# Optimization experiments

Measured on AMD Instinct MI355X. Metric: run time of the kernel, lower is better.

## Reference

```python
import jax, jax.numpy as jnp
import numpy as np

B, T, C = 64, 256, 64
E, H, HB, OUT = 32, 64, 128, 2


def setup_inputs() -> dict:
    key = jax.random.key(0)
    ks = iter(jax.random.split(key, 32))
    s = 0.02
    p = {}
    p["x"] = jax.random.normal(next(ks), (B, T, C), jnp.float32)
    # embedding Linear(1, E)
    p["embed_w"] = jax.random.normal(next(ks), (E, 1), jnp.float32) * s
    p["embed_b"] = jnp.zeros((E,), jnp.float32)
    # GRU (input E, hidden H); gate order r,z,n
    p["w_ih"] = jax.random.normal(next(ks), (3 * H, E), jnp.float32) * s
    p["w_hh"] = jax.random.normal(next(ks), (3 * H, H), jnp.float32) * s
    p["b_ih"] = jnp.zeros((3 * H,), jnp.float32)
    p["b_hh"] = jnp.zeros((3 * H,), jnp.float32)
    # BTP query / key MLPs: H->HB->HB->HB
    for nm in ("q", "k"):
        p[f"{nm}1_w"] = jax.random.normal(next(ks), (HB, H), jnp.float32) * s
        p[f"{nm}1_b"] = jnp.zeros((HB,), jnp.float32)
        p[f"{nm}2_w"] = jax.random.normal(next(ks), (HB, HB), jnp.float32) * s
        p[f"{nm}2_b"] = jnp.zeros((HB,), jnp.float32)
        p[f"{nm}3_w"] = jax.random.normal(next(ks), (HB, HB), jnp.float32) * s
        p[f"{nm}3_b"] = jnp.zeros((HB,), jnp.float32)
    # Gate bias (n_components x n_components), torch.randn init
    p["gate_bias"] = jax.random.normal(next(ks), (C, C), jnp.float32)
    # classifier: C^2 -> C^2/2 -> C^2/4 -> OUT
    d0, d1, d2 = C * C, C * C // 2, C * C // 4
    p["clf1_w"] = jax.random.normal(next(ks), (d1, d0), jnp.float32) * s
    p["clf1_b"] = jnp.zeros((d1,), jnp.float32)
    p["clf2_w"] = jax.random.normal(next(ks), (d2, d1), jnp.float32) * s
    p["clf2_b"] = jnp.zeros((d2,), jnp.float32)
    p["clf3_w"] = jax.random.normal(next(ks), (OUT, d2), jnp.float32) * s
    p["clf3_b"] = jnp.zeros((OUT,), jnp.float32)
    # predictor Linear(H, 1)
    p["pred_w"] = jax.random.normal(next(ks), (1, H), jnp.float32) * s
    p["pred_b"] = jnp.zeros((1,), jnp.float32)
    return p


def _mlp3(h, w1, b1, w2, b2, w3, b3):
    h = jax.nn.relu(h @ w1.T + b1)
    h = jax.nn.relu(h @ w2.T + b2)
    return h @ w3.T + b3


def reference(x, embed_w, embed_b, w_ih, w_hh, b_ih, b_hh,
              q1_w, q1_b, q2_w, q2_b, q3_w, q3_b,
              k1_w, k1_b, k2_w, k2_b, k3_w, k3_b,
              gate_bias, clf1_w, clf1_b, clf2_w, clf2_b, clf3_w, clf3_b,
              pred_w, pred_b):
    Bb, Tt, Cc = x.shape
    Hh = w_hh.shape[1]
    # embeddings: Linear(1,E) applied to each scalar -> [B,C,T,E]
    embedded = x.transpose(0, 2, 1)[..., None] * embed_w[:, 0] + embed_b
    xs = jnp.moveaxis(embedded, 2, 0)  # [T,B,C,E]

    def gru_cell(h, xt):
        gi = xt @ w_ih.T + b_ih           # [B,C,3H]
        gh = h @ w_hh.T + b_hh
        gi_r, gi_z, gi_n = jnp.split(gi, 3, axis=-1)
        gh_r, gh_z, gh_n = jnp.split(gh, 3, axis=-1)
        r = jax.nn.sigmoid(gi_r + gh_r)
        z = jax.nn.sigmoid(gi_z + gh_z)
        n = jnp.tanh(gi_n + r * gh_n)
        return (1.0 - z) * n + z * h

    def btp(h):
        q = _mlp3(h, q1_w, q1_b, q2_w, q2_b, q3_w, q3_b)   # [B,C,HB]
        k = _mlp3(h, k1_w, k1_b, k2_w, k2_b, k3_w, k3_b)
        transfer = jnp.einsum('bqd,bkd->bqk', q, k)        # [B,C,C]
        norms = jnp.sqrt(jnp.sum(transfer * transfer, axis=(1, 2), keepdims=True))
        transfer = transfer / norms
        gate = jax.nn.sigmoid(jnp.abs(transfer) + gate_bias)
        transfer = transfer * gate
        next_states = jnp.einsum('bij,bjd->bid', transfer, h)
        return next_states, transfer

    def step(h, xt):
        h = gru_cell(h, xt)
        h, transfer = btp(h)
        return h, (h, transfer)

    h0 = jnp.zeros((Bb, Cc, Hh), x.dtype)
    _, (hs, mats) = jax.lax.scan(step, h0, xs)
    hidden_states = jnp.moveaxis(hs, 0, 1)    # [B,T,C,H]
    matrices = jnp.moveaxis(mats, 0, 1)       # [B,T,C,C]

    # predictor on hidden states at t=0..T-2 -> predicts x[:,1:,:]
    predicted = (hidden_states[:, :-1] @ pred_w.T + pred_b)[..., 0]  # [B,T-1,C]

    clf_in = matrices.reshape(Bb, Tt, Cc * Cc)
    h1 = jax.nn.relu(clf_in @ clf1_w.T + clf1_b)   # dropout is identity in eval
    h2 = jax.nn.relu(h1 @ clf2_w.T + clf2_b)
    time_logits = h2 @ clf3_w.T + clf3_b            # [B,T,OUT]
    logits = jnp.mean(time_logits, axis=1)          # [B,OUT]
    return logits, matrices, time_logits, predicted, x[:, 1:, :]
```

## Files before the change

kernel.cpp:

```cpp
#include <hip/hip_runtime.h>
#include <hip/hip_bf16.h>
#include <math.h>

#define B_BATCH 64
#define T_STEPS 256
#define C_COMP  64

#define WSW_BYTE_OFF 2048
#define WHH_OFF 0
#define Q1_OFF 12288
#define K1_OFF 20480
#define Q2_OFF 28672
#define K2_OFF 45056
#define Q3_OFF 61440
#define K3_OFF 77824
#define C1WB_BYTE 262144
#define C2WB_BYTE 17039360
#define H1B_BYTE  21233664
#define H2B_BYTE  88342528
#define MB16_BYTE 121896960ULL

#define MAT_OFF  128
#define TL_OFF   67108992
#define PRED_OFF 67141760
#define XC_OFF   68186240

#define GST 196
#define HS  68
#define TS  68
#define GBS 68

typedef __attribute__((ext_vector_type(8))) short short8;
typedef __attribute__((ext_vector_type(4))) float f32x4;
#define MFMA16(a,b,c) __builtin_amdgcn_mfma_f32_16x16x32_bf16(a,b,c,0,0,0)

__device__ __forceinline__ float fsigm(float v) {
    return __builtin_amdgcn_rcpf(1.0f + __expf(-v));
}
__device__ __forceinline__ float ftanh(float v) {
    return 1.0f - 2.0f * __builtin_amdgcn_rcpf(__expf(2.0f * v) + 1.0f);
}
__device__ __forceinline__ short f2bs(float f) {
    unsigned u = __float_as_uint(f);
    u += 0x7fffu + ((u >> 16) & 1u);
    return (short)(u >> 16);
}
__device__ __forceinline__ float bf2f(short s) {
    return __uint_as_float(((unsigned)(unsigned short)s) << 16);
}
__device__ __forceinline__ unsigned pk2(float a, float b) {
    return (unsigned)(unsigned short)f2bs(a) | ((unsigned)(unsigned short)f2bs(b) << 16);
}
__device__ __forceinline__ void bar_lds() {
    asm volatile("s_waitcnt lgkmcnt(0)" ::: "memory");
    __builtin_amdgcn_s_barrier();
}
__device__ __forceinline__ int xorr(int row) { return ((row >> 1) & 7) << 3; }

__device__ __forceinline__ void async16(void* lds, const void* g) {
    __builtin_amdgcn_global_load_lds((const __attribute__((address_space(1))) void*)g,
                                     (__attribute__((address_space(3))) void*)lds, 16, 0, 0);
}

__global__ void precompute_kernel(const float* __restrict__ w_ih,
                                  const float* __restrict__ embed_w,
                                  const float* __restrict__ embed_b,
                                  const float* __restrict__ b_ih,
                                  float* __restrict__ avec, float* __restrict__ cvec)
{
    int g = threadIdx.x;
    if (g < 192) {
        float a = 0.f, c = 0.f;
        for (int e = 0; e < 32; ++e) {
            float w = w_ih[g * 32 + e];
            a += w * embed_w[e];
            c += w * embed_b[e];
        }
        avec[g] = a;
        cvec[g] = c + b_ih[g];
    }
}

__global__ void tobf16_kernel(const float* __restrict__ src, short* __restrict__ dst, int n)
{
    int i = blockIdx.x * 256 + threadIdx.x;
    if (i < n) dst[i] = f2bs(src[i]);
}

__global__ void expand_kernel(const short* __restrict__ mb, float* __restrict__ mat)
{
    const size_t i = ((size_t)blockIdx.x * 256 + threadIdx.x) * 8;
    short8 v = *(const short8*)&mb[i];
    float4 lo, hi;
    lo.x = bf2f(v[0]); lo.y = bf2f(v[1]); lo.z = bf2f(v[2]); lo.w = bf2f(v[3]);
    hi.x = bf2f(v[4]); hi.y = bf2f(v[5]); hi.z = bf2f(v[6]); hi.w = bf2f(v[7]);
    *reinterpret_cast<float4*>(&mat[i])     = lo;
    *reinterpret_cast<float4*>(&mat[i + 4]) = hi;
}

template<int KST, int AST, bool RELU>
__device__ __forceinline__ void two_strip_sw(
    const short* __restrict__ A,
    const short8* __restrict__ B0, const short8* __restrict__ B1,
    const f32x4 bias0, const f32x4 bias1,
    short* __restrict__ outb, const int s0, const int s1, const int ln, const int lh)
{
    f32x4 acc0[4], acc1[4];
#pragma unroll
    for (int g = 0; g < 4; ++g) { acc0[g] = bias0; acc1[g] = bias1; }
#pragma unroll
    for (int kk = 0; kk < KST; ++kk)
#pragma unroll
        for (int g = 0; g < 4; ++g) {
            const int row = g * 16 + ln;
            short8 a = *(const short8*)&A[row * AST + ((kk * 32 + lh * 8) ^ xorr(row))];
            acc0[g] = MFMA16(B0[kk], a, acc0[g]);
            acc1[g] = MFMA16(B1[kk], a, acc1[g]);
        }
#pragma unroll
    for (int g = 0; g < 4; ++g) {
        const int row = g * 16 + ln;
        f32x4 v0 = acc0[g], v1 = acc1[g];
        if (RELU) {
#pragma unroll
            for (int q = 0; q < 4; ++q) { v0[q] = fmaxf(v0[q], 0.f); v1[q] = fmaxf(v1[q], 0.f); }
        }
        uint2 p0, p1;
        p0.x = pk2(v0[0], v0[1]); p0.y = pk2(v0[2], v0[3]);
        p1.x = pk2(v1[0], v1[1]); p1.y = pk2(v1[2], v1[3]);
        *(uint2*)&outb[row * 128 + ((s0 * 16 + lh * 4) ^ xorr(row))] = p0;
        *(uint2*)&outb[row * 128 + ((s1 * 16 + lh * 4) ^ xorr(row))] = p1;
    }
}

__global__ __launch_bounds__(512) void scan_kernel(
    const float* __restrict__ x, const float* __restrict__ b_hh,
    const float* __restrict__ avec, const float* __restrict__ cvec,
    const short* __restrict__ wsw,
    const float* __restrict__ q1b, const float* __restrict__ q2b, const float* __restrict__ q3b,
    const float* __restrict__ k1b, const float* __restrict__ k2b, const float* __restrict__ k3b,
    const float* __restrict__ gate_bias,
    const float* __restrict__ pred_w, const float* __restrict__ pred_b,
    float* __restrict__ matrices, float* __restrict__ predicted,
    short* __restrict__ mb16, const int use_mb16)
{
    __shared__ __align__(16) short hb  [64 * 64];
    __shared__ __align__(16) short hbN [64 * 64];
    __shared__ __align__(16) short hbT [64 * 64];
    __shared__ __align__(16) float h32 [64 * HS];
    __shared__ __align__(16) short qf  [64 * 128];
    __shared__ __align__(16) short kf  [64 * 128];
    __shared__ __align__(16) float gbias_s[64 * GBS];
    __shared__ __align__(16) char arena[65536];
    __shared__ __align__(16) float avec_s[192];
    __shared__ __align__(16) float cvec_s[192];
    __shared__ __align__(16) float bhh_s[192];
    __shared__ __align__(16) float pw_s[64];
    __shared__ __align__(16) float xrow[64];
    __shared__ __align__(16) float red[8];

    float* gates = (float*)arena;
    short* act2q = (short*)arena;
    short* act2k = (short*)(arena + 16384);
    short* act1q = (short*)(arena + 32768);
    short* act1k = (short*)(arena + 49152);
    float* tf    = (float*)arena;
    short* tb    = (short*)(arena + 20480);

    const int tid = threadIdx.x;
    const int b = blockIdx.x;
    const int w = tid >> 6, lane = tid & 63;
    const int ln = lane & 15, lh = lane >> 4;
    const int path = w >> 2;
    const int wq = w & 3;

    for (int i = tid; i < 64 * 64; i += 512) { hb[i] = 0; hbN[i] = 0; hbT[i] = 0; }
    for (int i = tid; i < 64 * HS; i += 512) h32[i] = 0.f;
    for (int i = tid; i < 4096; i += 512)
        gbias_s[(i >> 6) * GBS + (i & 63)] = gate_bias[i];
    if (tid < 192) { avec_s[tid] = avec[tid]; cvec_s[tid] = cvec[tid]; bhh_s[tid] = b_hh[tid]; }
    if (tid < 64) { pw_s[tid] = pred_w[tid]; xrow[tid] = x[(size_t)b * T_STEPS * 64 + tid]; }
    const float pbv = pred_b[0];

    const short* whh_b = wsw + WHH_OFF;
    const short* l1w = path ? wsw + K1_OFF : wsw + Q1_OFF;
    const short* l2w = path ? wsw + K2_OFF : wsw + Q2_OFF;
    const short* l3w = path ? wsw + K3_OFF : wsw + Q3_OFF;
    const float* l1b = path ? k1b : q1b;
    const float* l2b = path ? k2b : q2b;
    const float* l3b = path ? k3b : q3b;

    short8 Bg[2][2], B1[2][2], B2[2][4], B3[2][4];
#pragma unroll
    for (int kk = 0; kk < 2; ++kk)
        Bg[0][kk] = *(const short8*)&whh_b[(w * 16 + ln) * 64 + kk * 32 + lh * 8];
    if (w < 4) {
#pragma unroll
        for (int kk = 0; kk < 2; ++kk)
            Bg[1][kk] = *(const short8*)&whh_b[((w + 8) * 16 + ln) * 64 + kk * 32 + lh * 8];
    }
#pragma unroll
    for (int s = 0; s < 2; ++s) {
        const int strip = wq + s * 4;
#pragma unroll
        for (int kk = 0; kk < 2; ++kk)
            B1[s][kk] = *(const short8*)&l1w[(strip * 16 + ln) * 64 + kk * 32 + lh * 8];
#pragma unroll
        for (int kk = 0; kk < 4; ++kk) {
            B2[s][kk] = *(const short8*)&l2w[(strip * 16 + ln) * 128 + kk * 32 + lh * 8];
            B3[s][kk] = *(const short8*)&l3w[(strip * 16 + ln) * 128 + kk * 32 + lh * 8];
        }
    }
    const f32x4 b1v0 = *(const f32x4*)&l1b[wq * 16 + lh * 4];
    const f32x4 b1v1 = *(const f32x4*)&l1b[(wq + 4) * 16 + lh * 4];
    const f32x4 b2v0 = *(const f32x4*)&l2b[wq * 16 + lh * 4];
    const f32x4 b2v1 = *(const f32x4*)&l2b[(wq + 4) * 16 + lh * 4];
    const f32x4 b3v0 = *(const f32x4*)&l3b[wq * 16 + lh * 4];
    const f32x4 b3v1 = *(const f32x4*)&l3b[(wq + 4) * 16 + lh * 4];
    __syncthreads();

    for (int t = 0; t < T_STEPS; ++t) {
        float xnext = 0.f;
        if (tid < 64 && t + 1 < T_STEPS)
            xnext = x[((size_t)b * T_STEPS + t + 1) * 64 + tid];
        if (t > 0) {
            const int c = tid >> 3, j0 = (tid & 7) * 8;
            f32x4 h0 = *(const f32x4*)&h32[c * HS + j0];
            f32x4 h1 = *(const f32x4*)&h32[c * HS + j0 + 4];
            f32x4 w0 = *(const f32x4*)&pw_s[j0];
            f32x4 w1 = *(const f32x4*)&pw_s[j0 + 4];
            float p = 0.f;
#pragma unroll
            for (int q = 0; q < 4; ++q) p = fmaf(h0[q], w0[q], fmaf(h1[q], w1[q], p));
            p += __shfl_xor(p, 1); p += __shfl_xor(p, 2); p += __shfl_xor(p, 4);
            if ((lane & 7) == 0)
                predicted[((size_t)b * (T_STEPS - 1) + (t - 1)) * 64 + c] = p + pbv;
        }
        {
            f32x4 accA[4], accB[4];
            const f32x4 bhA = *(const f32x4*)&bhh_s[w * 16 + lh * 4];
#pragma unroll
            for (int g = 0; g < 4; ++g) accA[g] = bhA;
            if (w < 4) {
                const f32x4 bhB = *(const f32x4*)&bhh_s[(w + 8) * 16 + lh * 4];
#pragma unroll
                for (int g = 0; g < 4; ++g) accB[g] = bhB;
            }
#pragma unroll
            for (int kk = 0; kk < 2; ++kk)
#pragma unroll
                for (int g = 0; g < 4; ++g) {
                    const int row = g * 16 + ln;
                    short8 hv = *(const short8*)&hb[row * 64 + ((kk * 32 + lh * 8) ^ xorr(row))];
                    accA[g] = MFMA16(Bg[0][kk], hv, accA[g]);
                    if (w < 4) accB[g] = MFMA16(Bg[1][kk], hv, accB[g]);
                }
#pragma unroll
            for (int g = 0; g < 4; ++g)
                *(f32x4*)&gates[(g * 16 + ln) * GST + w * 16 + lh * 4] = accA[g];
            if (w < 4) {
#pragma unroll
                for (int g = 0; g < 4; ++g)
                    *(f32x4*)&gates[(g * 16 + ln) * GST + (w + 8) * 16 + lh * 4] = accB[g];
            }
        }
        bar_lds();

        {
            const int c = tid >> 3, j0 = (tid & 7) * 8;
            const float xv = xrow[c];
            unsigned pk[4];
#pragma unroll
            for (int h2 = 0; h2 < 2; ++h2) {
                const int jh = j0 + h2 * 4;
                f32x4 gr4 = *(const f32x4*)&gates[c * GST + jh];
                f32x4 gz4 = *(const f32x4*)&gates[c * GST + 64 + jh];
                f32x4 gn4 = *(const f32x4*)&gates[c * GST + 128 + jh];
                f32x4 ho4 = *(const f32x4*)&h32[c * HS + jh];
                f32x4 ar4 = *(const f32x4*)&avec_s[jh];
                f32x4 az4 = *(const f32x4*)&avec_s[64 + jh];
                f32x4 an4 = *(const f32x4*)&avec_s[128 + jh];
                f32x4 cr4 = *(const f32x4*)&cvec_s[jh];
                f32x4 cz4 = *(const f32x4*)&cvec_s[64 + jh];
                f32x4 cn4 = *(const f32x4*)&cvec_s[128 + jh];
                f32x4 hn4;
#pragma unroll
                for (int q = 0; q < 4; ++q) {
                    const float r = fsigm(gr4[q] + fmaf(xv, ar4[q], cr4[q]));
                    const float z = fsigm(gz4[q] + fmaf(xv, az4[q], cz4[q]));
                    const float n = ftanh(fmaf(r, gn4[q], fmaf(xv, an4[q], cn4[q])));
                    hn4[q] = fmaf(z, ho4[q] - n, n);
                }
                *(f32x4*)&h32[c * HS + jh] = hn4;
                const unsigned plo = pk2(hn4[0], hn4[1]);
                const unsigned phi = pk2(hn4[2], hn4[3]);
                pk[h2 * 2] = plo; pk[h2 * 2 + 1] = phi;
                hbT[(jh + 0) * 64 + (c ^ xorr(jh + 0))] = (short)plo;
                hbT[(jh + 1) * 64 + (c ^ xorr(jh + 1))] = (short)(plo >> 16);
                hbT[(jh + 2) * 64 + (c ^ xorr(jh + 2))] = (short)phi;
                hbT[(jh + 3) * 64 + (c ^ xorr(jh + 3))] = (short)(phi >> 16);
            }
            uint4 pv; pv.x = pk[0]; pv.y = pk[1]; pv.z = pk[2]; pv.w = pk[3];
            *(uint4*)&hbN[c * 64 + (j0 ^ xorr(c))] = pv;
        }
        bar_lds();

        two_strip_sw<2, 64,  true >(hbN, B1[0], B1[1], b1v0, b1v1,
                                    path ? act1k : act1q, wq, wq + 4, ln, lh);
        bar_lds();
        two_strip_sw<4, 128, true >(path ? act1k : act1q, B2[0], B2[1], b2v0, b2v1,
                                    path ? act2k : act2q, wq, wq + 4, ln, lh);
        bar_lds();
        two_strip_sw<4, 128, false>(path ? act2k : act2q, B3[0], B3[1], b3v0, b3v1,
                                    path ? kf : qf, wq, wq + 4, ln, lh);
        bar_lds();

        {
            const int qg = w & 3, kg = (w >> 2) * 2;
            f32x4 ac0 = {0,0,0,0}, ac1 = {0,0,0,0};
#pragma unroll
            for (int kk = 0; kk < 4; ++kk) {
                const int rq = qg * 16 + ln, rk0 = kg * 16 + ln, rk1 = (kg + 1) * 16 + ln;
                short8 bq = *(const short8*)&qf[rq * 128 + ((kk * 32 + lh * 8) ^ xorr(rq))];
                short8 a0 = *(const short8*)&kf[rk0 * 128 + ((kk * 32 + lh * 8) ^ xorr(rk0))];
                short8 a1 = *(const short8*)&kf[rk1 * 128 + ((kk * 32 + lh * 8) ^ xorr(rk1))];
                ac0 = MFMA16(a0, bq, ac0);
                ac1 = MFMA16(a1, bq, ac1);
            }
            const int qrow = qg * 16 + ln;
            *(f32x4*)&tf[qrow * TS + kg * 16 + lh * 4]       = ac0;
            *(f32x4*)&tf[qrow * TS + (kg + 1) * 16 + lh * 4] = ac1;
            float ss = 0.f;
#pragma unroll
            for (int q = 0; q < 4; ++q)
                ss = fmaf(ac0[q], ac0[q], fmaf(ac1[q], ac1[q], ss));
#pragma unroll
            for (int off = 1; off < 64; off <<= 1) ss += __shfl_xor(ss, off);
            if (lane == 0) red[w] = ss;
            if (tid < 64 && t + 1 < T_STEPS) xrow[tid] = xnext;
        }
        bar_lds();

        {
            const int ci = tid >> 3, j0 = (tid & 7) * 8;
            const float ssum = red[0]+red[1]+red[2]+red[3]+red[4]+red[5]+red[6]+red[7];
            const float inv = __builtin_amdgcn_rsqf(ssum);
            const size_t mbase = ((size_t)b * T_STEPS + t) * 4096;
            unsigned pk[4];
#pragma unroll
            for (int h2 = 0; h2 < 2; ++h2) {
                const int jh = j0 + h2 * 4;
                f32x4 t4  = *(const f32x4*)&tf[ci * TS + jh];
                f32x4 gb4 = *(const f32x4*)&gbias_s[ci * GBS + jh];
                f32x4 v4;
#pragma unroll
                for (int q = 0; q < 4; ++q) {
                    const float tv = t4[q] * inv;
                    const float g = fsigm(fabsf(tv) + gb4[q]);
                    v4[q] = tv * g;
                }
                pk[h2 * 2]     = pk2(v4[0], v4[1]);
                pk[h2 * 2 + 1] = pk2(v4[2], v4[3]);
                if (!use_mb16)
                    *(f32x4*)&matrices[mbase + ci * 64 + jh] = v4;
            }
            uint4 pv; pv.x = pk[0]; pv.y = pk[1]; pv.z = pk[2]; pv.w = pk[3];
            if (use_mb16)
                *(uint4*)&mb16[mbase + ci * 64 + j0] = pv;
            *(uint4*)&tb[ci * 64 + (j0 ^ xorr(ci))] = pv;
        }
        bar_lds();

        {
            const int jg = w & 3, ig = (w >> 2) * 2;
            f32x4 hc0 = {0,0,0,0}, hc1 = {0,0,0,0};
#pragma unroll
            for (int kk = 0; kk < 2; ++kk) {
                const int rj = jg * 16 + ln, ri0 = ig * 16 + ln, ri1 = (ig + 1) * 16 + ln;
                short8 bt = *(const short8*)&tb [rj * 64 + ((kk * 32 + lh * 8) ^ xorr(rj))];
                short8 a0 = *(const short8*)&hbT[ri0 * 64 + ((kk * 32 + lh * 8) ^ xorr(ri0))];
                short8 a1 = *(const short8*)&hbT[ri1 * 64 + ((kk * 32 + lh * 8) ^ xorr(ri1))];
                hc0 = MFMA16(a0, bt, hc0);
                hc1 = MFMA16(a1, bt, hc1);
            }
            const int row = jg * 16 + ln;
            *(f32x4*)&h32[row * HS + ig * 16 + lh * 4]       = hc0;
            *(f32x4*)&h32[row * HS + (ig + 1) * 16 + lh * 4] = hc1;
            uint2 p0, p1;
            p0.x = pk2(hc0[0], hc0[1]); p0.y = pk2(hc0[2], hc0[3]);
            p1.x = pk2(hc1[0], hc1[1]); p1.y = pk2(hc1[2], hc1[3]);
            *(uint2*)&hb[row * 64 + ((ig * 16 + lh * 4) ^ xorr(row))]       = p0;
            *(uint2*)&hb[row * 64 + (((ig + 1) * 16 + lh * 4) ^ xorr(row))] = p1;
        }
        bar_lds();
    }
}

__global__ void copyx_kernel(const float* __restrict__ x, float* __restrict__ out5)
{
    int i = blockIdx.x * 256 + threadIdx.x;
    if (i < B_BATCH * (T_STEPS - 1) * C_COMP) {
        int b = i / ((T_STEPS - 1) * C_COMP);
        int r = i - b * (T_STEPS - 1) * C_COMP;
        out5[i] = x[(size_t)b * (T_STEPS * C_COMP) + r + C_COMP];
    }
}

__global__ __launch_bounds__(256) void gemm1_kernel(
    const float* __restrict__ A, const short* __restrict__ Bw,
    const float* __restrict__ bias, short* __restrict__ Cb,
    const int M, const int N, const int K)
{
    __shared__ __align__(16) short Asb[128 * 64];
    __shared__ __align__(16) short Bsb[128 * 64];
    const int tid = threadIdx.x;
    const int w = tid >> 6, lane = tid & 63;
    const int ln = lane & 15, lh = lane >> 4;
    const int wr = w >> 1, wc = w & 1;

    const int ntc = N >> 7;
    const int g = blockIdx.x;
    const int xcd = g & 7, chunk = g >> 3;
    const int mt = xcd * ((M >> 7) >> 3) + chunk / ntc;
    const int nt = chunk % ntc;
    const int m0 = mt << 7, n0 = nt << 7;

    const int ar = tid >> 1;
    const int ac = (tid & 1) << 5;
    const short* bsrc = Bw + (size_t)(n0 + w * 32 + (lane >> 3)) * K + ((lane & 7) << 3);
    short* bdst = &Bsb[w * 32 * 64 + lane * 8];

    f32x4 acc[4][4];
#pragma unroll
    for (int m = 0; m < 4; ++m)
#pragma unroll
        for (int n = 0; n < 4; ++n) acc[m][n] = (f32x4){0, 0, 0, 0};

    for (int k0 = 0; k0 < K; k0 += 64) {
        const float* arow = A + (size_t)(m0 + ar) * K + k0 + ac;
        float4 av[8];
#pragma unroll
        for (int i = 0; i < 8; ++i) av[i] = *reinterpret_cast<const float4*>(arow + i * 4);
        short8 cv[4];
#pragma unroll
        for (int i = 0; i < 4; ++i) {
            cv[i][0] = f2bs(av[2*i].x);   cv[i][1] = f2bs(av[2*i].y);
            cv[i][2] = f2bs(av[2*i].z);   cv[i][3] = f2bs(av[2*i].w);
            cv[i][4] = f2bs(av[2*i+1].x); cv[i][5] = f2bs(av[2*i+1].y);
            cv[i][6] = f2bs(av[2*i+1].z); cv[i][7] = f2bs(av[2*i+1].w);
        }
        __syncthreads();
#pragma unroll
        for (int i = 0; i < 4; ++i)
            *reinterpret_cast<short8*>(&Asb[ar * 64 + ac + i * 8]) = cv[i];
#pragma unroll
        for (int i = 0; i < 4; ++i)
            async16(bdst + i * 512, bsrc + (size_t)i * 8 * K + k0);
        __syncthreads();
#pragma unroll
        for (int kk = 0; kk < 2; ++kk) {
            short8 af[4], bfr[4];
#pragma unroll
            for (int m = 0; m < 4; ++m)
                af[m] = *reinterpret_cast<const short8*>(&Asb[(wr*64 + m*16 + ln)*64 + kk*32 + lh*8]);
#pragma unroll
            for (int n = 0; n < 4; ++n)
                bfr[n] = *reinterpret_cast<const short8*>(&Bsb[(wc*64 + n*16 + ln)*64 + kk*32 + lh*8]);
#pragma unroll
            for (int m = 0; m < 4; ++m)
#pragma unroll
                for (int n = 0; n < 4; ++n)
                    acc[m][n] = MFMA16(af[m], bfr[n], acc[m][n]);
        }
    }
#pragma unroll
    for (int n = 0; n < 4; ++n) {
        const int col = n0 + wc * 64 + n * 16 + ln;
        const float bv = bias[col];
#pragma unroll
        for (int m = 0; m < 4; ++m)
#pragma unroll
            for (int q = 0; q < 4; ++q) {
                const int row = m0 + wr * 64 + m * 16 + lh * 4 + q;
                Cb[(size_t)row * N + col] = f2bs(fmaxf(acc[m][n][q] + bv, 0.f));
            }
    }
}

__global__ __launch_bounds__(256) void gemm2_kernel(
    const short* __restrict__ Ab, const short* __restrict__ Bw,
    const float* __restrict__ bias, short* __restrict__ Cb,
    const int M, const int N, const int K)
{
    __shared__ __align__(16) short Asb[128 * 64];
    __shared__ __align__(16) short Bsb[128 * 64];
    const int tid = threadIdx.x;
    const int w = tid >> 6, lane = tid & 63;
    const int ln = lane & 15, lh = lane >> 4;
    const int wr = w >> 1, wc = w & 1;

    const int ntc = N >> 7;
    const int g = blockIdx.x;
    const int xcd = g & 7, chunk = g >> 3;
    const int mt = xcd * ((M >> 7) >> 3) + chunk / ntc;
    const int nt = chunk % ntc;
    const int m0 = mt << 7, n0 = nt << 7;

    const short* asrc = Ab + (size_t)(m0 + w * 32 + (lane >> 3)) * K + ((lane & 7) << 3);
    const short* bsrc = Bw + (size_t)(n0 + w * 32 + (lane >> 3)) * K + ((lane & 7) << 3);
    short* adst = &Asb[w * 32 * 64 + lane * 8];
    short* bdst = &Bsb[w * 32 * 64 + lane * 8];

    f32x4 acc[4][4];
#pragma unroll
    for (int m = 0; m < 4; ++m)
#pragma unroll
        for (int n = 0; n < 4; ++n) acc[m][n] = (f32x4){0, 0, 0, 0};

    for (int k0 = 0; k0 < K; k0 += 64) {
        __syncthreads();
#pragma unroll
        for (int i = 0; i < 4; ++i) {
            async16(adst + i * 512, asrc + (size_t)i * 8 * K + k0);
            async16(bdst + i * 512, bsrc + (size_t)i * 8 * K + k0);
        }
        __syncthreads();
#pragma unroll
        for (int kk = 0; kk < 2; ++kk) {
            short8 af[4], bfr[4];
#pragma unroll
            for (int m = 0; m < 4; ++m)
                af[m] = *reinterpret_cast<const short8*>(&Asb[(wr*64 + m*16 + ln)*64 + kk*32 + lh*8]);
#pragma unroll
            for (int n = 0; n < 4; ++n)
                bfr[n] = *reinterpret_cast<const short8*>(&Bsb[(wc*64 + n*16 + ln)*64 + kk*32 + lh*8]);
#pragma unroll
            for (int m = 0; m < 4; ++m)
#pragma unroll
                for (int n = 0; n < 4; ++n)
                    acc[m][n] = MFMA16(af[m], bfr[n], acc[m][n]);
        }
    }
#pragma unroll
    for (int n = 0; n < 4; ++n) {
        const int col = n0 + wc * 64 + n * 16 + ln;
        const float bv = bias[col];
#pragma unroll
        for (int m = 0; m < 4; ++m)
#pragma unroll
            for (int q = 0; q < 4; ++q) {
                const int row = m0 + wr * 64 + m * 16 + lh * 4 + q;
                Cb[(size_t)row * N + col] = f2bs(fmaxf(acc[m][n][q] + bv, 0.f));
            }
    }
}

__global__ __launch_bounds__(256) void clf3_kernel(const short* __restrict__ h2b,
    const float* __restrict__ w3, const float* __restrict__ b3, float* __restrict__ TL)
{
    const int lane = threadIdx.x & 63;
    const int w = threadIdx.x >> 6;
    const size_t r = (size_t)blockIdx.x * 4 + w;
    const short* hr = h2b + r * 1024;
    float a0 = 0.f, a1 = 0.f;
#pragma unroll
    for (int half = 0; half < 2; ++half) {
        const int k = half * 512 + lane * 8;
        short8 hv = *(const short8*)&hr[k];
#pragma unroll
        for (int u = 0; u < 8; ++u) {
            const float hf = bf2f(hv[u]);
            a0 = fmaf(hf, w3[k + u], a0);
            a1 = fmaf(hf, w3[1024 + k + u], a1);
        }
    }
    for (int off = 32; off; off >>= 1) { a0 += __shfl_xor(a0, off); a1 += __shfl_xor(a1, off); }
    if (lane == 0) {
        TL[r * 2 + 0] = a0 + b3[0];
        TL[r * 2 + 1] = a1 + b3[1];
    }
}

__global__ void logits_kernel(const float* __restrict__ TL, float* __restrict__ out)
{
    const int tid = threadIdx.x;
    if (tid >= 128) return;
    const int b = tid >> 1, o = tid & 1;
    float s = 0.f;
    for (int t = 0; t < T_STEPS; ++t) s += TL[((size_t)b * T_STEPS + t) * 2 + o];
    out[b * 2 + o] = s * (1.0f / 256.0f);
}

extern "C" void kernel_launch(void* const* d_in, const int* in_sizes, int n_in,
                              void* d_out, int out_size, void* d_ws, size_t ws_size,
                              hipStream_t stream)
{
    const float* x       = (const float*)d_in[0];
    const float* embed_w = (const float*)d_in[1];
    const float* embed_b = (const float*)d_in[2];
    const float* w_ih    = (const float*)d_in[3];
    const float* w_hh    = (const float*)d_in[4];
    const float* b_ih    = (const float*)d_in[5];
    const float* b_hh    = (const float*)d_in[6];
    const float* q1w = (const float*)d_in[7],  *q1b = (const float*)d_in[8];
    const float* q2w = (const float*)d_in[9],  *q2b = (const float*)d_in[10];
    const float* q3w = (const float*)d_in[11], *q3b = (const float*)d_in[12];
    const float* k1w = (const float*)d_in[13], *k1b = (const float*)d_in[14];
    const float* k2w = (const float*)d_in[15], *k2b = (const float*)d_in[16];
    const float* k3w = (const float*)d_in[17], *k3b = (const float*)d_in[18];
    const float* gate_bias = (const float*)d_in[19];
    const float* c1w = (const float*)d_in[20], *c1b = (const float*)d_in[21];
    const float* c2w = (const float*)d_in[22], *c2b = (const float*)d_in[23];
    const float* c3w = (const float*)d_in[24], *c3b = (const float*)d_in[25];
    const float* pw  = (const float*)d_in[26], *pb  = (const float*)d_in[27];

    float* out       = (float*)d_out;
    float* logits    = out;
    float* matrices  = out + MAT_OFF;
    float* TL        = out + TL_OFF;
    float* predicted = out + PRED_OFF;
    float* xcopy     = out + XC_OFF;

    float* ws   = (float*)d_ws;
    float* avec = ws;
    float* cvec = ws + 192;
    short* wsw  = (short*)((char*)d_ws + WSW_BYTE_OFF);
    short* c1wb = (short*)((char*)d_ws + C1WB_BYTE);
    short* c2wb = (short*)((char*)d_ws + C2WB_BYTE);
    short* h1b  = (short*)((char*)d_ws + H1B_BYTE);
    short* h2b  = (short*)((char*)d_ws + H2B_BYTE);

    const int use_mb16 = (ws_size >= MB16_BYTE + 134217728ULL) ? 1 : 0;
    short* mb16 = use_mb16 ? (short*)((char*)d_ws + MB16_BYTE) : (short*)d_ws;

    precompute_kernel<<<1, 256, 0, stream>>>(w_ih, embed_w, embed_b, b_ih, avec, cvec);

    tobf16_kernel<<<(12288 + 255) / 256, 256, 0, stream>>>(w_hh, wsw + WHH_OFF, 12288);
    tobf16_kernel<<<(8192  + 255) / 256, 256, 0, stream>>>(q1w,  wsw + Q1_OFF,  8192);
    tobf16_kernel<<<(8192  + 255) / 256, 256, 0, stream>>>(k1w,  wsw + K1_OFF,  8192);
    tobf16_kernel<<<(16384 + 255) / 256, 256, 0, stream>>>(q2w,  wsw + Q2_OFF,  16384);
    tobf16_kernel<<<(16384 + 255) / 256, 256, 0, stream>>>(k2w,  wsw + K2_OFF,  16384);
    tobf16_kernel<<<(16384 + 255) / 256, 256, 0, stream>>>(q3w,  wsw + Q3_OFF,  16384);
    tobf16_kernel<<<(16384 + 255) / 256, 256, 0, stream>>>(k3w,  wsw + K3_OFF,  16384);
    tobf16_kernel<<<(2048 * 4096 + 255) / 256, 256, 0, stream>>>(c1w, c1wb, 2048 * 4096);
    tobf16_kernel<<<(1024 * 2048 + 255) / 256, 256, 0, stream>>>(c2w, c2wb, 1024 * 2048);

    scan_kernel<<<B_BATCH, 512, 0, stream>>>(x, b_hh, avec, cvec, wsw,
        q1b, q2b, q3b, k1b, k2b, k3b, gate_bias, pw, pb, matrices, predicted,
        mb16, use_mb16);

    if (use_mb16)
        expand_kernel<<<32768, 256, 0, stream>>>(mb16, matrices);

    copyx_kernel<<<(B_BATCH * (T_STEPS - 1) * C_COMP + 255) / 256, 256, 0, stream>>>(x, xcopy);

    const int Mtot = B_BATCH * T_STEPS;
    if (use_mb16) {
        gemm2_kernel<<<(Mtot / 128) * (2048 / 128), 256, 0, stream>>>(
            mb16, c1wb, c1b, h1b, Mtot, 2048, 4096);
    } else {
        gemm1_kernel<<<(Mtot / 128) * (2048 / 128), 256, 0, stream>>>(
            matrices, c1wb, c1b, h1b, Mtot, 2048, 4096);
    }
    gemm2_kernel<<<(Mtot / 128) * (1024 / 128), 256, 0, stream>>>(
        h1b, c2wb, c2b, h2b, Mtot, 1024, 2048);
    clf3_kernel<<<Mtot / 4, 256, 0, stream>>>(h2b, c3w, c3b, TL);
    logits_kernel<<<1, 128, 0, stream>>>(TL, logits);
}
```

Measured before the change: 2.770 ms.

## Fuse scan and classifier GEMMs into persistent kernel with atomic job queue

```diff
diff --git a/kernel.cpp b/kernel.cpp
--- a/kernel.cpp
+++ b/kernel.cpp
@@ -6,7 +6,8 @@
 #define T_STEPS 256
 #define C_COMP  64
 
-#define WSW_BYTE_OFF 2048
+#define CTRL_BYTE 2048
+#define WSW_BYTE_OFF 4096
 #define WHH_OFF 0
 #define Q1_OFF 12288
 #define K1_OFF 20480
@@ -30,6 +31,8 @@
 #define TS  68
 #define GBS 68
 
+#define NJOB 3328
+
 typedef __attribute__((ext_vector_type(8))) short short8;
 typedef __attribute__((ext_vector_type(4))) float f32x4;
 #define MFMA16(a,b,c) __builtin_amdgcn_mfma_f32_16x16x32_bf16(a,b,c,0,0,0)
@@ -60,6 +63,24 @@
 __device__ __forceinline__ void async16(void* lds, const void* g) {
     __builtin_amdgcn_global_load_lds((const __attribute__((address_space(1))) void*)g,
                                      (__attribute__((address_space(3))) void*)lds, 16, 0, 0);
+}
+__device__ __forceinline__ int aload_acq(int* p) {
+    return __hip_atomic_load(p, __ATOMIC_ACQUIRE, __HIP_MEMORY_SCOPE_AGENT);
+}
+__device__ __forceinline__ void astore_rel(int* p, int v) {
+    __hip_atomic_store(p, v, __ATOMIC_RELEASE, __HIP_MEMORY_SCOPE_AGENT);
+}
+__device__ __forceinline__ int aadd_rel(int* p, int v) {
+    return __hip_atomic_fetch_add(p, v, __ATOMIC_RELEASE, __HIP_MEMORY_SCOPE_AGENT);
+}
+__device__ __forceinline__ int aadd_rlx(int* p, int v) {
+    return __hip_atomic_fetch_add(p, v, __ATOMIC_RELAXED, __HIP_MEMORY_SCOPE_AGENT);
+}
+__device__ __forceinline__ void wait_ge(int* p, int need) {
+    if (threadIdx.x == 0) {
+        while (aload_acq(p) < need) __builtin_amdgcn_s_sleep(127);
+    }
+    __syncthreads();
 }
 
 __global__ void precompute_kernel(const float* __restrict__ w_ih,
@@ -98,6 +119,101 @@
     *reinterpret_cast<float4*>(&mat[i + 4]) = hi;
 }
 
+__global__ void copyx_kernel(const float* __restrict__ x, float* __restrict__ out5)
+{
+    int i = blockIdx.x * 256 + threadIdx.x;
+    if (i < B_BATCH * (T_STEPS - 1) * C_COMP) {
+        int b = i / ((T_STEPS - 1) * C_COMP);
+        int r = i - b * (T_STEPS - 1) * C_COMP;
+        out5[i] = x[(size_t)b * (T_STEPS * C_COMP) + r + C_COMP];
+    }
+}
+
+template<bool AF32>
+__device__ __forceinline__ void gemm_tile_512(
+    const void* Aptr, const short* __restrict__ Bw, const float* __restrict__ bias,
+    short* __restrict__ Cb, const size_t row0, const int n0,
+    const int N, const int K, short* Asb, short* Bsb)
+{
+    const int tid = threadIdx.x;
+    const int w = tid >> 6, lane = tid & 63;
+    const int ln = lane & 15, lh = lane >> 4;
+    const int wr = w >> 2, wc = w & 3;
+
+    const short* Ab = (const short*)Aptr;
+    const float* Af = (const float*)Aptr;
+
+    f32x4 acc[4][2];
+#pragma unroll
+    for (int m = 0; m < 4; ++m) {
+        acc[m][0] = (f32x4){0, 0, 0, 0};
+        acc[m][1] = (f32x4){0, 0, 0, 0};
+    }
+
+    for (int k0 = 0; k0 < K; k0 += 64) {
+        if (AF32) {
+            const int ar = tid >> 2, ac = (tid & 3) << 4;
+            const float* arow = Af + (row0 + ar) * (size_t)K + k0 + ac;
+            float4 av[4];
+#pragma unroll
+            for (int i = 0; i < 4; ++i) av[i] = *reinterpret_cast<const float4*>(arow + i * 4);
+            short8 cv[2];
+#pragma unroll
+            for (int i = 0; i < 2; ++i) {
+                cv[i][0] = f2bs(av[2*i].x);   cv[i][1] = f2bs(av[2*i].y);
+                cv[i][2] = f2bs(av[2*i].z);   cv[i][3] = f2bs(av[2*i].w);
+                cv[i][4] = f2bs(av[2*i+1].x); cv[i][5] = f2bs(av[2*i+1].y);
+                cv[i][6] = f2bs(av[2*i+1].z); cv[i][7] = f2bs(av[2*i+1].w);
+            }
+            __syncthreads();
+            *reinterpret_cast<short8*>(&Asb[ar * 64 + ac])     = cv[0];
+            *reinterpret_cast<short8*>(&Asb[ar * 64 + ac + 8]) = cv[1];
+#pragma unroll
+            for (int i = 0; i < 2; ++i)
+                async16(&Bsb[w * 1024 + i * 512 + lane * 8],
+                        Bw + (size_t)(n0 + w * 16 + i * 8 + (lane >> 3)) * K + k0 + ((lane & 7) << 3));
+            __syncthreads();
+        } else {
+            __syncthreads();
+#pragma unroll
+            for (int i = 0; i < 2; ++i) {
+                async16(&Asb[w * 1024 + i * 512 + lane * 8],
+                        Ab + (row0 + w * 16 + i * 8 + (lane >> 3)) * (size_t)K + k0 + ((lane & 7) << 3));
+                async16(&Bsb[w * 1024 + i * 512 + lane * 8],
+                        Bw + (size_t)(n0 + w * 16 + i * 8 + (lane >> 3)) * K + k0 + ((lane & 7) << 3));
+            }
+            __syncthreads();
+        }
+#pragma unroll
+        for (int kk = 0; kk < 2; ++kk) {
+            short8 af[4], bfr[2];
+#pragma unroll
+            for (int m = 0; m < 4; ++m)
+                af[m] = *reinterpret_cast<const short8*>(&Asb[(wr*64 + m*16 + ln)*64 + kk*32 + lh*8]);
+#pragma unroll
+            for (int n = 0; n < 2; ++n)
+                bfr[n] = *reinterpret_cast<const short8*>(&Bsb[(wc*32 + n*16 + ln)*64 + kk*32 + lh*8]);
+#pragma unroll
+            for (int m = 0; m < 4; ++m)
+#pragma unroll
+                for (int n = 0; n < 2; ++n)
+                    acc[m][n] = MFMA16(af[m], bfr[n], acc[m][n]);
+        }
+    }
+#pragma unroll
+    for (int n = 0; n < 2; ++n) {
+        const int col = n0 + wc * 32 + n * 16 + ln;
+        const float bv = bias[col];
+#pragma unroll
+        for (int m = 0; m < 4; ++m)
+#pragma unroll
+            for (int q = 0; q < 4; ++q) {
+                const size_t row = row0 + wr * 64 + m * 16 + lh * 4 + q;
+                Cb[row * N + col] = f2bs(fmaxf(acc[m][n][q] + bv, 0.f));
+            }
+    }
+}
+
 template<int KST, int AST, bool RELU>
 __device__ __forceinline__ void two_strip_sw(
     const short* __restrict__ A,
@@ -133,7 +249,7 @@
     }
 }
 
-__global__ __launch_bounds__(512) void scan_kernel(
+__global__ __launch_bounds__(512) void fused_kernel(
     const float* __restrict__ x, const float* __restrict__ b_hh,
     const float* __restrict__ avec, const float* __restrict__ cvec,
     const short* __restrict__ wsw,
@@ -142,7 +258,12 @@
     const float* __restrict__ gate_bias,
     const float* __restrict__ pred_w, const float* __restrict__ pred_b,
     float* __restrict__ matrices, float* __restrict__ predicted,
-    short* __restrict__ mb16, const int use_mb16)
+    short* __restrict__ mb16, const int use_mb16,
+    const short* __restrict__ c1wb, const float* __restrict__ c1b,
+    const short* __restrict__ c2wb, const float* __restrict__ c2b,
+    const float* __restrict__ c3w, const float* __restrict__ c3b,
+    short* __restrict__ h1b, short* __restrict__ h2b, float* __restrict__ TL,
+    int* __restrict__ ctrl, const int persist)
 {
     __shared__ __align__(16) short hb  [64 * 64];
     __shared__ __align__(16) short hbN [64 * 64];
@@ -158,251 +279,328 @@
     __shared__ __align__(16) float pw_s[64];
     __shared__ __align__(16) float xrow[64];
     __shared__ __align__(16) float red[8];
-
-    float* gates = (float*)arena;
-    short* act2q = (short*)arena;
-    short* act2k = (short*)(arena + 16384);
-    short* act1q = (short*)(arena + 32768);
-    short* act1k = (short*)(arena + 49152);
-    float* tf    = (float*)arena;
-    short* tb    = (short*)(arena + 20480);
+    __shared__ int jslot;
 
     const int tid = threadIdx.x;
-    const int b = blockIdx.x;
+    const int bid = blockIdx.x;
     const int w = tid >> 6, lane = tid & 63;
     const int ln = lane & 15, lh = lane >> 4;
-    const int path = w >> 2;
-    const int wq = w & 3;
-
-    for (int i = tid; i < 64 * 64; i += 512) { hb[i] = 0; hbN[i] = 0; hbT[i] = 0; }
-    for (int i = tid; i < 64 * HS; i += 512) h32[i] = 0.f;
-    for (int i = tid; i < 4096; i += 512)
-        gbias_s[(i >> 6) * GBS + (i & 63)] = gate_bias[i];
-    if (tid < 192) { avec_s[tid] = avec[tid]; cvec_s[tid] = cvec[tid]; bhh_s[tid] = b_hh[tid]; }
-    if (tid < 64) { pw_s[tid] = pred_w[tid]; xrow[tid] = x[(size_t)b * T_STEPS * 64 + tid]; }
-    const float pbv = pred_b[0];
-
-    const short* whh_b = wsw + WHH_OFF;
-    const short* l1w = path ? wsw + K1_OFF : wsw + Q1_OFF;
-    const short* l2w = path ? wsw + K2_OFF : wsw + Q2_OFF;
-    const short* l3w = path ? wsw + K3_OFF : wsw + Q3_OFF;
-    const float* l1b = path ? k1b : q1b;
-    const float* l2b = path ? k2b : q2b;
-    const float* l3b = path ? k3b : q3b;
-
-    short8 Bg[2][2], B1[2][2], B2[2][4], B3[2][4];
-#pragma unroll
-    for (int kk = 0; kk < 2; ++kk)
-        Bg[0][kk] = *(const short8*)&whh_b[(w * 16 + ln) * 64 + kk * 32 + lh * 8];
-    if (w < 4) {
+
+    int* qhead = ctrl;
+    int* prog  = ctrl + 16;
+    int* done1 = ctrl + 96;
+    int* done2 = ctrl + 224;
+
+    if (bid < 64) {
+        float* gates = (float*)arena;
+        short* act2q = (short*)arena;
+        short* act2k = (short*)(arena + 16384);
+        short* act1q = (short*)(arena + 32768);
+        short* act1k = (short*)(arena + 49152);
+        float* tf    = (float*)arena;
+        short* tb    = (short*)(arena + 20480);
+
+        const int b = bid;
+        const int path = w >> 2;
+        const int wq = w & 3;
+
+        for (int i = tid; i < 64 * 64; i += 512) { hb[i] = 0; hbN[i] = 0; hbT[i] = 0; }
+        for (int i = tid; i < 64 * HS; i += 512) h32[i] = 0.f;
+        for (int i = tid; i < 4096; i += 512)
+            gbias_s[(i >> 6) * GBS + (i & 63)] = gate_bias[i];
+        if (tid < 192) { avec_s[tid] = avec[tid]; cvec_s[tid] = cvec[tid]; bhh_s[tid] = b_hh[tid]; }
+        if (tid < 64) { pw_s[tid] = pred_w[tid]; xrow[tid] = x[(size_t)b * T_STEPS * 64 + tid]; }
+        const float pbv = pred_b[0];
+
+        const short* whh_b = wsw + WHH_OFF;
+        const short* l1w = path ? wsw + K1_OFF : wsw + Q1_OFF;
+        const short* l2w = path ? wsw + K2_OFF : wsw + Q2_OFF;
+        const short* l3w = path ? wsw + K3_OFF : wsw + Q3_OFF;
+        const float* l1b = path ? k1b : q1b;
+        const float* l2b = path ? k2b : q2b;
+        const float* l3b = path ? k3b : q3b;
+
+        short8 Bg[2][2], B1[2][2], B2[2][4], B3[2][4];
 #pragma unroll
         for (int kk = 0; kk < 2; ++kk)
-            Bg[1][kk] = *(const short8*)&whh_b[((w + 8) * 16 + ln) * 64 + kk * 32 + lh * 8];
-    }
-#pragma unroll
-    for (int s = 0; s < 2; ++s) {
-        const int strip = wq + s * 4;
-#pragma unroll
-        for (int kk = 0; kk < 2; ++kk)
-            B1[s][kk] = *(const short8*)&l1w[(strip * 16 + ln) * 64 + kk * 32 + lh * 8];
-#pragma unroll
-        for (int kk = 0; kk < 4; ++kk) {
-            B2[s][kk] = *(const short8*)&l2w[(strip * 16 + ln) * 128 + kk * 32 + lh * 8];
-            B3[s][kk] = *(const short8*)&l3w[(strip * 16 + ln) * 128 + kk * 32 + lh * 8];
-        }
-    }
-    const f32x4 b1v0 = *(const f32x4*)&l1b[wq * 16 + lh * 4];
-    const f32x4 b1v1 = *(const f32x4*)&l1b[(wq + 4) * 16 + lh * 4];
-    const f32x4 b2v0 = *(const f32x4*)&l2b[wq * 16 + lh * 4];
-    const f32x4 b2v1 = *(const f32x4*)&l2b[(wq + 4) * 16 + lh * 4];
-    const f32x4 b3v0 = *(const f32x4*)&l3b[wq * 16 + lh * 4];
-    const f32x4 b3v1 = *(const f32x4*)&l3b[(wq + 4) * 16 + lh * 4];
-    __syncthreads();
-
-    for (int t = 0; t < T_STEPS; ++t) {
-        float xnext = 0.f;
-        if (tid < 64 && t + 1 < T_STEPS)
-            xnext = x[((size_t)b * T_STEPS + t + 1) * 64 + tid];
-        if (t > 0) {
-            const int c = tid >> 3, j0 = (tid & 7) * 8;
-            f32x4 h0 = *(const f32x4*)&h32[c * HS + j0];
-            f32x4 h1 = *(const f32x4*)&h32[c * HS + j0 + 4];
-            f32x4 w0 = *(const f32x4*)&pw_s[j0];
-            f32x4 w1 = *(const f32x4*)&pw_s[j0 + 4];
-            float p = 0.f;
-#pragma unroll
-            for (int q = 0; q < 4; ++q) p = fmaf(h0[q], w0[q], fmaf(h1[q], w1[q], p));
-            p += __shfl_xor(p, 1); p += __shfl_xor(p, 2); p += __shfl_xor(p, 4);
-            if ((lane & 7) == 0)
-                predicted[((size_t)b * (T_STEPS - 1) + (t - 1)) * 64 + c] = p + pbv;
-        }
-        {
-            f32x4 accA[4], accB[4];
-            const f32x4 bhA = *(const f32x4*)&bhh_s[w * 16 + lh * 4];
-#pragma unroll
-            for (int g = 0; g < 4; ++g) accA[g] = bhA;
-            if (w < 4) {
-                const f32x4 bhB = *(const f32x4*)&bhh_s[(w + 8) * 16 + lh * 4];
-#pragma unroll
-                for (int g = 0; g < 4; ++g) accB[g] = bhB;
-            }
+            Bg[0][kk] = *(const short8*)&whh_b[(w * 16 + ln) * 64 + kk * 32 + lh * 8];
+        if (w < 4) {
 #pragma unroll
             for (int kk = 0; kk < 2; ++kk)
-#pragma unroll
-                for (int g = 0; g < 4; ++g) {
-                    const int row = g * 16 + ln;
-                    short8 hv = *(const short8*)&hb[row * 64 + ((kk * 32 + lh * 8) ^ xorr(row))];
-                    accA[g] = MFMA16(Bg[0][kk], hv, accA[g]);
-                    if (w < 4) accB[g] = MFMA16(Bg[1][kk], hv, accB[g]);
+                Bg[1][kk] = *(const short8*)&whh_b[((w + 8) * 16 + ln) * 64 + kk * 32 + lh * 8];
+        }
+#pragma unroll
+        for (int s = 0; s < 2; ++s) {
+            const int strip = wq + s * 4;
+#pragma unroll
+            for (int kk = 0; kk < 2; ++kk)
+                B1[s][kk] = *(const short8*)&l1w[(strip * 16 + ln) * 64 + kk * 32 + lh * 8];
+#pragma unroll
+            for (int kk = 0; kk < 4; ++kk) {
+                B2[s][kk] = *(const short8*)&l2w[(strip * 16 + ln) * 128 + kk * 32 + lh * 8];
+                B3[s][kk] = *(const short8*)&l3w[(strip * 16 + ln) * 128 + kk * 32 + lh * 8];
+            }
+        }
+        const f32x4 b1v0 = *(const f32x4*)&l1b[wq * 16 + lh * 4];
+        const f32x4 b1v1 = *(const f32x4*)&l1b[(wq + 4) * 16 + lh * 4];
+        const f32x4 b2v0 = *(const f32x4*)&l2b[wq * 16 + lh * 4];
+        const f32x4 b2v1 = *(const f32x4*)&l2b[(wq + 4) * 16 + lh * 4];
+        const f32x4 b3v0 = *(const f32x4*)&l3b[wq * 16 + lh * 4];
+        const f32x4 b3v1 = *(const f32x4*)&l3b[(wq + 4) * 16 + lh * 4];
+        __syncthreads();
+
+        for (int t = 0; t < T_STEPS; ++t) {
+            float xnext = 0.f;
+            if (tid < 64 && t + 1 < T_STEPS)
+                xnext = x[((size_t)b * T_STEPS + t + 1) * 64 + tid];
+            if (t > 0) {
+                const int c = tid >> 3, j0 = (tid & 7) * 8;
+                f32x4 h0 = *(const f32x4*)&h32[c * HS + j0];
+                f32x4 h1 = *(const f32x4*)&h32[c * HS + j0 + 4];
+                f32x4 w0 = *(const f32x4*)&pw_s[j0];
+                f32x4 w1 = *(const f32x4*)&pw_s[j0 + 4];
+                float p = 0.f;
+#pragma unroll
+                for (int q = 0; q < 4; ++q) p = fmaf(h0[q], w0[q], fmaf(h1[q], w1[q], p));
+                p += __shfl_xor(p, 1); p += __shfl_xor(p, 2); p += __shfl_xor(p, 4);
+                if ((lane & 7) == 0)
+                    predicted[((size_t)b * (T_STEPS - 1) + (t - 1)) * 64 + c] = p + pbv;
+            }
+            {
+                f32x4 accA[4], accB[4];
+                const f32x4 bhA = *(const f32x4*)&bhh_s[w * 16 + lh * 4];
+#pragma unroll
+                for (int g = 0; g < 4; ++g) accA[g] = bhA;
+                if (w < 4) {
+                    const f32x4 bhB = *(const f32x4*)&bhh_s[(w + 8) * 16 + lh * 4];
+#pragma unroll
+                    for (int g = 0; g < 4; ++g) accB[g] = bhB;
                 }
 #pragma unroll
-            for (int g = 0; g < 4; ++g)
-                *(f32x4*)&gates[(g * 16 + ln) * GST + w * 16 + lh * 4] = accA[g];
-            if (w < 4) {
+                for (int kk = 0; kk < 2; ++kk)
+#pragma unroll
+                    for (int g = 0; g < 4; ++g) {
+                        const int row = g * 16 + ln;
+                        short8 hv = *(const short8*)&hb[row * 64 + ((kk * 32 + lh * 8) ^ xorr(row))];
+                        accA[g] = MFMA16(Bg[0][kk], hv, accA[g]);
+                        if (w < 4) accB[g] = MFMA16(Bg[1][kk], hv, accB[g]);
+                    }
 #pragma unroll
                 for (int g = 0; g < 4; ++g)
-                    *(f32x4*)&gates[(g * 16 + ln) * GST + (w + 8) * 16 + lh * 4] = accB[g];
-            }
-        }
-        bar_lds();
-
-        {
-            const int c = tid >> 3, j0 = (tid & 7) * 8;
-            const float xv = xrow[c];
-            unsigned pk[4];
-#pragma unroll
-            for (int h2 = 0; h2 < 2; ++h2) {
-                const int jh = j0 + h2 * 4;
-                f32x4 gr4 = *(const f32x4*)&gates[c * GST + jh];
-                f32x4 gz4 = *(const f32x4*)&gates[c * GST + 64 + jh];
-                f32x4 gn4 = *(const f32x4*)&gates[c * GST + 128 + jh];
-                f32x4 ho4 = *(const f32x4*)&h32[c * HS + jh];
-                f32x4 ar4 = *(const f32x4*)&avec_s[jh];
-                f32x4 az4 = *(const f32x4*)&avec_s[64 + jh];
-                f32x4 an4 = *(const f32x4*)&avec_s[128 + jh];
-                f32x4 cr4 = *(const f32x4*)&cvec_s[jh];
-                f32x4 cz4 = *(const f32x4*)&cvec_s[64 + jh];
-                f32x4 cn4 = *(const f32x4*)&cvec_s[128 + jh];
-                f32x4 hn4;
-#pragma unroll
-                for (int q = 0; q < 4; ++q) {
-                    const float r = fsigm(gr4[q] + fmaf(xv, ar4[q], cr4[q]));
-                    const float z = fsigm(gz4[q] + fmaf(xv, az4[q], cz4[q]));
-                    const float n = ftanh(fmaf(r, gn4[q], fmaf(xv, an4[q], cn4[q])));
-                    hn4[q] = fmaf(z, ho4[q] - n, n);
+                    *(f32x4*)&gates[(g * 16 + ln) * GST + w * 16 + lh * 4] = accA[g];
+                if (w < 4) {
+#pragma unroll
+                    for (int g = 0; g < 4; ++g)
+                        *(f32x4*)&gates[(g * 16 + ln) * GST + (w + 8) * 16 + lh * 4] = accB[g];
                 }
-                *(f32x4*)&h32[c * HS + jh] = hn4;
-                const unsigned plo = pk2(hn4[0], hn4[1]);
-                const unsigned phi = pk2(hn4[2], hn4[3]);
-                pk[h2 * 2] = plo; pk[h2 * 2 + 1] = phi;
-                hbT[(jh + 0) * 64 + (c ^ xorr(jh + 0))] = (short)plo;
-                hbT[(jh + 1) * 64 + (c ^ xorr(jh + 1))] = (short)(plo >> 16);
-                hbT[(jh + 2) * 64 + (c ^ xorr(jh + 2))] = (short)phi;
-                hbT[(jh + 3) * 64 + (c ^ xorr(jh + 3))] = (short)(phi >> 16);
-            }
-            uint4 pv; pv.x = pk[0]; pv.y = pk[1]; pv.z = pk[2]; pv.w = pk[3];
-            *(uint4*)&hbN[c * 64 + (j0 ^ xorr(c))] = pv;
-        }
-        bar_lds();
-
-        two_strip_sw<2, 64,  true >(hbN, B1[0], B1[1], b1v0, b1v1,
-                                    path ? act1k : act1q, wq, wq + 4, ln, lh);
-        bar_lds();
-        two_strip_sw<4, 128, true >(path ? act1k : act1q, B2[0], B2[1], b2v0, b2v1,
-                                    path ? act2k : act2q, wq, wq + 4, ln, lh);
-        bar_lds();
-        two_strip_sw<4, 128, false>(path ? act2k : act2q, B3[0], B3[1], b3v0, b3v1,
-                                    path ? kf : qf, wq, wq + 4, ln, lh);
-        bar_lds();
-
-        {
-            const int qg = w & 3, kg = (w >> 2) * 2;
-            f32x4 ac0 = {0,0,0,0}, ac1 = {0,0,0,0};
-#pragma unroll
-            for (int kk = 0; kk < 4; ++kk) {
-                const int rq = qg * 16 + ln, rk0 = kg * 16 + ln, rk1 = (kg + 1) * 16 + ln;
-                short8 bq = *(const short8*)&qf[rq * 128 + ((kk * 32 + lh * 8) ^ xorr(rq))];
-                short8 a0 = *(const short8*)&kf[rk0 * 128 + ((kk * 32 + lh * 8) ^ xorr(rk0))];
-                short8 a1 = *(const short8*)&kf[rk1 * 128 + ((kk * 32 + lh * 8) ^ xorr(rk1))];
-                ac0 = MFMA16(a0, bq, ac0);
-                ac1 = MFMA16(a1, bq, ac1);
-            }
-            const int qrow = qg * 16 + ln;
-            *(f32x4*)&tf[qrow * TS + kg * 16 + lh * 4]       = ac0;
-            *(f32x4*)&tf[qrow * TS + (kg + 1) * 16 + lh * 4] = ac1;
-            float ss = 0.f;
-#pragma unroll
-            for (int q = 0; q < 4; ++q)
-                ss = fmaf(ac0[q], ac0[q], fmaf(ac1[q], ac1[q], ss));
-#pragma unroll
-            for (int off = 1; off < 64; off <<= 1) ss += __shfl_xor(ss, off);
-            if (lane == 0) red[w] = ss;
-            if (tid < 64 && t + 1 < T_STEPS) xrow[tid] = xnext;
-        }
-        bar_lds();
-
-        {
-            const int ci = tid >> 3, j0 = (tid & 7) * 8;
-            const float ssum = red[0]+red[1]+red[2]+red[3]+red[4]+red[5]+red[6]+red[7];
-            const float inv = __builtin_amdgcn_rsqf(ssum);
-            const size_t mbase = ((size_t)b * T_STEPS + t) * 4096;
-            unsigned pk[4];
-#pragma unroll
-            for (int h2 = 0; h2 < 2; ++h2) {
-                const int jh = j0 + h2 * 4;
-                f32x4 t4  = *(const f32x4*)&tf[ci * TS + jh];
-                f32x4 gb4 = *(const f32x4*)&gbias_s[ci * GBS + jh];
-                f32x4 v4;
-#pragma unroll
-                for (int q = 0; q < 4; ++q) {
-                    const float tv = t4[q] * inv;
-                    const float g = fsigm(fabsf(tv) + gb4[q]);
-                    v4[q] = tv * g;
+            }
+            bar_lds();
+
+            {
+                const int c = tid >> 3, j0 = (tid & 7) * 8;
+                const float xv = xrow[c];
+                unsigned pk[4];
+#pragma unroll
+                for (int h2 = 0; h2 < 2; ++h2) {
+                    const int jh = j0 + h2 * 4;
+                    f32x4 gr4 = *(const f32x4*)&gates[c * GST + jh];
+                    f32x4 gz4 = *(const f32x4*)&gates[c * GST + 64 + jh];
+                    f32x4 gn4 = *(const f32x4*)&gates[c * GST + 128 + jh];
+                    f32x4 ho4 = *(const f32x4*)&h32[c * HS + jh];
+                    f32x4 ar4 = *(const f32x4*)&avec_s[jh];
+                    f32x4 az4 = *(const f32x4*)&avec_s[64 + jh];
+                    f32x4 an4 = *(const f32x4*)&avec_s[128 + jh];
+                    f32x4 cr4 = *(const f32x4*)&cvec_s[jh];
+                    f32x4 cz4 = *(const f32x4*)&cvec_s[64 + jh];
+                    f32x4 cn4 = *(const f32x4*)&cvec_s[128 + jh];
+                    f32x4 hn4;
+#pragma unroll
+                    for (int q = 0; q < 4; ++q) {
+                        const float r = fsigm(gr4[q] + fmaf(xv, ar4[q], cr4[q]));
+                        const float z = fsigm(gz4[q] + fmaf(xv, az4[q], cz4[q]));
+                        const float n = ftanh(fmaf(r, gn4[q], fmaf(xv, an4[q], cn4[q])));
+                        hn4[q] = fmaf(z, ho4[q] - n, n);
+                    }
+                    *(f32x4*)&h32[c * HS + jh] = hn4;
+                    const unsigned plo = pk2(hn4[0], hn4[1]);
+                    const unsigned phi = pk2(hn4[2], hn4[3]);
+                    pk[h2 * 2] = plo; pk[h2 * 2 + 1] = phi;
+                    hbT[(jh + 0) * 64 + (c ^ xorr(jh + 0))] = (short)plo;
+                    hbT[(jh + 1) * 64 + (c ^ xorr(jh + 1))] = (short)(plo >> 16);
+                    hbT[(jh + 2) * 64 + (c ^ xorr(jh + 2))] = (short)phi;
+                    hbT[(jh + 3) * 64 + (c ^ xorr(jh + 3))] = (short)(phi >> 16);
                 }
-                pk[h2 * 2]     = pk2(v4[0], v4[1]);
-                pk[h2 * 2 + 1] = pk2(v4[2], v4[3]);
-                if (!use_mb16)
-                    *(f32x4*)&matrices[mbase + ci * 64 + jh] = v4;
-            }
-            uint4 pv; pv.x = pk[0]; pv.y = pk[1]; pv.z = pk[2]; pv.w = pk[3];
+                uint4 pv; pv.x = pk[0]; pv.y = pk[1]; pv.z = pk[2]; pv.w = pk[3];
+                *(uint4*)&hbN[c * 64 + (j0 ^ xorr(c))] = pv;
+            }
+            bar_lds();
+
+            two_strip_sw<2, 64,  true >(hbN, B1[0], B1[1], b1v0, b1v1,
+                                        path ? act1k : act1q, wq, wq + 4, ln, lh);
+            bar_lds();
+            two_strip_sw<4, 128, true >(path ? act1k : act1q, B2[0], B2[1], b2v0, b2v1,
+                                        path ? act2k : act2q, wq, wq + 4, ln, lh);
+            bar_lds();
+            two_strip_sw<4, 128, false>(path ? act2k : act2q, B3[0], B3[1], b3v0, b3v1,
+                                        path ? kf : qf, wq, wq + 4, ln, lh);
+            bar_lds();
+
+            {
+                const int qg = w & 3, kg = (w >> 2) * 2;
+                f32x4 ac0 = {0,0,0,0}, ac1 = {0,0,0,0};
+#pragma unroll
+                for (int kk = 0; kk < 4; ++kk) {
+                    const int rq = qg * 16 + ln, rk0 = kg * 16 + ln, rk1 = (kg + 1) * 16 + ln;
+                    short8 bq = *(const short8*)&qf[rq * 128 + ((kk * 32 + lh * 8) ^ xorr(rq))];
+                    short8 a0 = *(const short8*)&kf[rk0 * 128 + ((kk * 32 + lh * 8) ^ xorr(rk0))];
+                    short8 a1 = *(const short8*)&kf[rk1 * 128 + ((kk * 32 + lh * 8) ^ xorr(rk1))];
+                    ac0 = MFMA16(a0, bq, ac0);
+                    ac1 = MFMA16(a1, bq, ac1);
+                }
+                const int qrow = qg * 16 + ln;
+                *(f32x4*)&tf[qrow * TS + kg * 16 + lh * 4]       = ac0;
+                *(f32x4*)&tf[qrow * TS + (kg + 1) * 16 + lh * 4] = ac1;
+                float ss = 0.f;
+#pragma unroll
+                for (int q = 0; q < 4; ++q)
+                    ss = fmaf(ac0[q], ac0[q], fmaf(ac1[q], ac1[q], ss));
+#pragma unroll
+                for (int off = 1; off < 64; off <<= 1) ss += __shfl_xor(ss, off);
+                if (lane == 0) red[w] = ss;
+                if (tid < 64 && t + 1 < T_STEPS) xrow[tid] = xnext;
+            }
+            bar_lds();
+
+            {
+                const int ci = tid >> 3, j0 = (tid & 7) * 8;
+                const float ssum = red[0]+red[1]+red[2]+red[3]+red[4]+red[5]+red[6]+red[7];
+                const float inv = __builtin_amdgcn_rsqf(ssum);
+                const size_t mbase = ((size_t)b * T_STEPS + t) * 4096;
+                unsigned pk[4];
+#pragma unroll
+                for (int h2 = 0; h2 < 2; ++h2) {
+                    const int jh = j0 + h2 * 4;
+                    f32x4 t4  = *(const f32x4*)&tf[ci * TS + jh];
+                    f32x4 gb4 = *(const f32x4*)&gbias_s[ci * GBS + jh];
+                    f32x4 v4;
+#pragma unroll
+                    for (int q = 0; q < 4; ++q) {
+                        const float tv = t4[q] * inv;
+                        const float g = fsigm(fabsf(tv) + gb4[q]);
+                        v4[q] = tv * g;
+                    }
+                    pk[h2 * 2]     = pk2(v4[0], v4[1]);
+                    pk[h2 * 2 + 1] = pk2(v4[2], v4[3]);
+                    if (!use_mb16)
+                        *(f32x4*)&matrices[mbase + ci * 64 + jh] = v4;
+                }
+                uint4 pv; pv.x = pk[0]; pv.y = pk[1]; pv.z = pk[2]; pv.w = pk[3];
+                if (use_mb16)
+                    *(uint4*)&mb16[mbase + ci * 64 + j0] = pv;
+                *(uint4*)&tb[ci * 64 + (j0 ^ xorr(ci))] = pv;
+            }
+            if (persist && (t & 31) == 31) {
+                __syncthreads();
+                if (tid == 0) astore_rel(&prog[b], t + 1);
+            } else {
+                bar_lds();
+            }
+
+            {
+                const int jg = w & 3, ig = (w >> 2) * 2;
+                f32x4 hc0 = {0,0,0,0}, hc1 = {0,0,0,0};
+#pragma unroll
+                for (int kk = 0; kk < 2; ++kk) {
+                    const int rj = jg * 16 + ln, ri0 = ig * 16 + ln, ri1 = (ig + 1) * 16 + ln;
+                    short8 bt = *(const short8*)&tb [rj * 64 + ((kk * 32 + lh * 8) ^ xorr(rj))];
+                    short8 a0 = *(const short8*)&hbT[ri0 * 64 + ((kk * 32 + lh * 8) ^ xorr(ri0))];
+                    short8 a1 = *(const short8*)&hbT[ri1 * 64 + ((kk * 32 + lh * 8) ^ xorr(ri1))];
+                    hc0 = MFMA16(a0, bt, hc0);
+                    hc1 = MFMA16(a1, bt, hc1);
+                }
+                const int row = jg * 16 + ln;
+                *(f32x4*)&h32[row * HS + ig * 16 + lh * 4]       = hc0;
+                *(f32x4*)&h32[row * HS + (ig + 1) * 16 + lh * 4] = hc1;
+                uint2 p0, p1;
+                p0.x = pk2(hc0[0], hc0[1]); p0.y = pk2(hc0[2], hc0[3]);
+                p1.x = pk2(hc1[0], hc1[1]); p1.y = pk2(hc1[2], hc1[3]);
+                *(uint2*)&hb[row * 64 + ((ig * 16 + lh * 4) ^ xorr(row))]       = p0;
+                *(uint2*)&hb[row * 64 + (((ig + 1) * 16 + lh * 4) ^ xorr(row))] = p1;
+            }
+            bar_lds();
+        }
+    }
+
+    if (!persist) return;
+
+    short* Asb = (short*)arena;
+    short* Bsb = (short*)(arena + 16384);
+
+    while (true) {
+        if (tid == 0) jslot = aadd_rlx(qhead, 1);
+        __syncthreads();
+        const int j = jslot;
+        if (j >= NJOB) break;
+        const int mt = j / 1664, rr = j % 1664;
+        if (rr < 64) {
+            if (use_mb16) {
+                const int bb = rr;
+                wait_ge(&prog[bb], (mt + 1) * 128);
+                const size_t r0 = (size_t)bb * 256 + (size_t)mt * 128;
+                for (int it = tid; it < 65536; it += 512) {
+                    const size_t e0 = r0 * 4096 + (size_t)it * 8;
+                    short8 v = *(const short8*)&mb16[e0];
+                    float4 lo, hi;
+                    lo.x = bf2f(v[0]); lo.y = bf2f(v[1]); lo.z = bf2f(v[2]); lo.w = bf2f(v[3]);
+                    hi.x = bf2f(v[4]); hi.y = bf2f(v[5]); hi.z = bf2f(v[6]); hi.w = bf2f(v[7]);
+                    *reinterpret_cast<float4*>(&matrices[e0])     = lo;
+                    *reinterpret_cast<float4*>(&matrices[e0 + 4]) = hi;
+                }
+            }
+        } else if (rr < 1088) {
+            const int i = rr - 64, bb = i >> 4, nt = i & 15;
+            wait_ge(&prog[bb], (mt + 1) * 128);
+            const size_t r0 = (size_t)bb * 256 + (size_t)mt * 128;
             if (use_mb16)
-                *(uint4*)&mb16[mbase + ci * 64 + j0] = pv;
-            *(uint4*)&tb[ci * 64 + (j0 ^ xorr(ci))] = pv;
-        }
-        bar_lds();
-
-        {
-            const int jg = w & 3, ig = (w >> 2) * 2;
-            f32x4 hc0 = {0,0,0,0}, hc1 = {0,0,0,0};
-#pragma unroll
-            for (int kk = 0; kk < 2; ++kk) {
-                const int rj = jg * 16 + ln, ri0 = ig * 16 + ln, ri1 = (ig + 1) * 16 + ln;
-                short8 bt = *(const short8*)&tb [rj * 64 + ((kk * 32 + lh * 8) ^ xorr(rj))];
-                short8 a0 = *(const short8*)&hbT[ri0 * 64 + ((kk * 32 + lh * 8) ^ xorr(ri0))];
-                short8 a1 = *(const short8*)&hbT[ri1 * 64 + ((kk * 32 + lh * 8) ^ xorr(ri1))];
-                hc0 = MFMA16(a0, bt, hc0);
-                hc1 = MFMA16(a1, bt, hc1);
-            }
-            const int row = jg * 16 + ln;
-            *(f32x4*)&h32[row * HS + ig * 16 + lh * 4]       = hc0;
-            *(f32x4*)&h32[row * HS + (ig + 1) * 16 + lh * 4] = hc1;
-            uint2 p0, p1;
-            p0.x = pk2(hc0[0], hc0[1]); p0.y = pk2(hc0[2], hc0[3]);
-            p1.x = pk2(hc1[0], hc1[1]); p1.y = pk2(hc1[2], hc1[3]);
-            *(uint2*)&hb[row * 64 + ((ig * 16 + lh * 4) ^ xorr(row))]       = p0;
-            *(uint2*)&hb[row * 64 + (((ig + 1) * 16 + lh * 4) ^ xorr(row))] = p1;
-        }
-        bar_lds();
-    }
-}
-
-__global__ void copyx_kernel(const float* __restrict__ x, float* __restrict__ out5)
-{
-    int i = blockIdx.x * 256 + threadIdx.x;
-    if (i < B_BATCH * (T_STEPS - 1) * C_COMP) {
-        int b = i / ((T_STEPS - 1) * C_COMP);
-        int r = i - b * (T_STEPS - 1) * C_COMP;
-        out5[i] = x[(size_t)b * (T_STEPS * C_COMP) + r + C_COMP];
+                gemm_tile_512<false>(mb16, c1wb, c1b, h1b, r0, nt * 128, 2048, 4096, Asb, Bsb);
+            else
+                gemm_tile_512<true >(matrices, c1wb, c1b, h1b, r0, nt * 128, 2048, 4096, Asb, Bsb);
+            __syncthreads();
+            if (tid == 0) aadd_rel(&done1[bb * 2 + mt], 1);
+        } else if (rr < 1600) {
+            const int i = rr - 1088, bb = i >> 3, nt = i & 7;
+            wait_ge(&done1[bb * 2 + mt], 16);
+            const size_t r0 = (size_t)bb * 256 + (size_t)mt * 128;
+            gemm_tile_512<false>(h1b, c2wb, c2b, h2b, r0, nt * 128, 1024, 2048, Asb, Bsb);
+            __syncthreads();
+            if (tid == 0) aadd_rel(&done2[bb * 2 + mt], 1);
+        } else {
+            const int bb = rr - 1600;
+            wait_ge(&done2[bb * 2 + mt], 8);
+            const size_t r0 = (size_t)bb * 256 + (size_t)mt * 128;
+            for (int pass = 0; pass < 16; ++pass) {
+                const size_t row = r0 + pass * 8 + w;
+                const short* hr = h2b + row * 1024;
+                float a0 = 0.f, a1 = 0.f;
+#pragma unroll
+                for (int half = 0; half < 2; ++half) {
+                    const int k = half * 512 + lane * 8;
+                    short8 hv = *(const short8*)&hr[k];
+#pragma unroll
+                    for (int u = 0; u < 8; ++u) {
+                        const float hf = bf2f(hv[u]);
+                        a0 = fmaf(hf, c3w[k + u], a0);
+                        a1 = fmaf(hf, c3w[1024 + k + u], a1);
+                    }
+                }
+                for (int off = 32; off; off >>= 1) { a0 += __shfl_xor(a0, off); a1 += __shfl_xor(a1, off); }
+                if (lane == 0) {
+                    TL[row * 2 + 0] = a0 + c3b[0];
+                    TL[row * 2 + 1] = a1 + c3b[1];
+                }
+            }
+        }
+        __syncthreads();
     }
 }
 
@@ -417,25 +615,21 @@
     const int w = tid >> 6, lane = tid & 63;
     const int ln = lane & 15, lh = lane >> 4;
     const int wr = w >> 1, wc = w & 1;
-
     const int ntc = N >> 7;
     const int g = blockIdx.x;
     const int xcd = g & 7, chunk = g >> 3;
     const int mt = xcd * ((M >> 7) >> 3) + chunk / ntc;
     const int nt = chunk % ntc;
     const int m0 = mt << 7, n0 = nt << 7;
-
     const int ar = tid >> 1;
     const int ac = (tid & 1) << 5;
     const short* bsrc = Bw + (size_t)(n0 + w * 32 + (lane >> 3)) * K + ((lane & 7) << 3);
     short* bdst = &Bsb[w * 32 * 64 + lane * 8];
-
     f32x4 acc[4][4];
 #pragma unroll
     for (int m = 0; m < 4; ++m)
 #pragma unroll
         for (int n = 0; n < 4; ++n) acc[m][n] = (f32x4){0, 0, 0, 0};
-
     for (int k0 = 0; k0 < K; k0 += 64) {
         const float* arow = A + (size_t)(m0 + ar) * K + k0 + ac;
         float4 av[8];
@@ -498,25 +692,21 @@
     const int w = tid >> 6, lane = tid & 63;
     const int ln = lane & 15, lh = lane >> 4;
     const int wr = w >> 1, wc = w & 1;
-
     const int ntc = N >> 7;
     const int g = blockIdx.x;
     const int xcd = g & 7, chunk = g >> 3;
     const int mt = xcd * ((M >> 7) >> 3) + chunk / ntc;
     const int nt = chunk % ntc;
     const int m0 = mt << 7, n0 = nt << 7;
-
     const short* asrc = Ab + (size_t)(m0 + w * 32 + (lane >> 3)) * K + ((lane & 7) << 3);
     const short* bsrc = Bw + (size_t)(n0 + w * 32 + (lane >> 3)) * K + ((lane & 7) << 3);
     short* adst = &Asb[w * 32 * 64 + lane * 8];
     short* bdst = &Bsb[w * 32 * 64 + lane * 8];
-
     f32x4 acc[4][4];
 #pragma unroll
     for (int m = 0; m < 4; ++m)
 #pragma unroll
         for (int n = 0; n < 4; ++n) acc[m][n] = (f32x4){0, 0, 0, 0};
-
     for (int k0 = 0; k0 < K; k0 += 64) {
         __syncthreads();
 #pragma unroll
@@ -624,6 +814,7 @@
     float* ws   = (float*)d_ws;
     float* avec = ws;
     float* cvec = ws + 192;
+    int*   ctrl = (int*)((char*)d_ws + CTRL_BYTE);
     short* wsw  = (short*)((char*)d_ws + WSW_BYTE_OFF);
     short* c1wb = (short*)((char*)d_ws + C1WB_BYTE);
     short* c2wb = (short*)((char*)d_ws + C2WB_BYTE);
@@ -632,6 +823,10 @@
 
     const int use_mb16 = (ws_size >= MB16_BYTE + 134217728ULL) ? 1 : 0;
     short* mb16 = use_mb16 ? (short*)((char*)d_ws + MB16_BYTE) : (short*)d_ws;
+
+    int dev = 0; hipGetDevice(&dev);
+    int mp = 0; hipDeviceGetAttribute(&mp, hipDeviceAttributeMultiprocessorCount, dev);
+    const int persist = (mp >= 256) ? 1 : 0;
 
     precompute_kernel<<<1, 256, 0, stream>>>(w_ih, embed_w, embed_b, b_ih, avec, cvec);
 
@@ -645,25 +840,29 @@
     tobf16_kernel<<<(2048 * 4096 + 255) / 256, 256, 0, stream>>>(c1w, c1wb, 2048 * 4096);
     tobf16_kernel<<<(1024 * 2048 + 255) / 256, 256, 0, stream>>>(c2w, c2wb, 1024 * 2048);
 
-    scan_kernel<<<B_BATCH, 512, 0, stream>>>(x, b_hh, avec, cvec, wsw,
-        q1b, q2b, q3b, k1b, k2b, k3b, gate_bias, pw, pb, matrices, predicted,
-        mb16, use_mb16);
-
-    if (use_mb16)
-        expand_kernel<<<32768, 256, 0, stream>>>(mb16, matrices);
-
     copyx_kernel<<<(B_BATCH * (T_STEPS - 1) * C_COMP + 255) / 256, 256, 0, stream>>>(x, xcopy);
 
-    const int Mtot = B_BATCH * T_STEPS;
-    if (use_mb16) {
-        gemm2_kernel<<<(Mtot / 128) * (2048 / 128), 256, 0, stream>>>(
-            mb16, c1wb, c1b, h1b, Mtot, 2048, 4096);
-    } else {
-        gemm1_kernel<<<(Mtot / 128) * (2048 / 128), 256, 0, stream>>>(
-            matrices, c1wb, c1b, h1b, Mtot, 2048, 4096);
-    }
-    gemm2_kernel<<<(Mtot / 128) * (1024 / 128), 256, 0, stream>>>(
-        h1b, c2wb, c2b, h2b, Mtot, 1024, 2048);
-    clf3_kernel<<<Mtot / 4, 256, 0, stream>>>(h2b, c3w, c3b, TL);
+    if (persist)
+        hipMemsetAsync(ctrl, 0, 2048, stream);
+
+    fused_kernel<<<persist ? 256 : 64, 512, 0, stream>>>(
+        x, b_hh, avec, cvec, wsw, q1b, q2b, q3b, k1b, k2b, k3b,
+        gate_bias, pw, pb, matrices, predicted, mb16, use_mb16,
+        c1wb, c1b, c2wb, c2b, c3w, c3b, h1b, h2b, TL, ctrl, persist);
+
+    if (!persist) {
+        const int Mtot = B_BATCH * T_STEPS;
+        if (use_mb16) {
+            expand_kernel<<<32768, 256, 0, stream>>>(mb16, matrices);
+            gemm2_kernel<<<(Mtot / 128) * (2048 / 128), 256, 0, stream>>>(
+                mb16, c1wb, c1b, h1b, Mtot, 2048, 4096);
+        } else {
+            gemm1_kernel<<<(Mtot / 128) * (2048 / 128), 256, 0, stream>>>(
+                matrices, c1wb, c1b, h1b, Mtot, 2048, 4096);
+        }
+        gemm2_kernel<<<(Mtot / 128) * (1024 / 128), 256, 0, stream>>>(
+            h1b, c2wb, c2b, h2b, Mtot, 1024, 2048);
+        clf3_kernel<<<Mtot / 4, 256, 0, stream>>>(h2b, c3w, c3b, TL);
+    }
     logits_kernel<<<1, 128, 0, stream>>>(TL, logits);
 }
```

After: 2.967 ms. 7.1% more time.
